# Optimization experiments

Measured on AMD Instinct MI355X. Metric: run time of the kernel, lower is better.

## Reference

```python
import jax, jax.numpy as jnp
import numpy as np

B, S, D_IN, D_OUT = 4, 2048, 1024, 1024

def setup_inputs() -> dict:
    key = jax.random.key(0)
    k0, k1, k2, k3 = jax.random.split(key, 4)
    sc = 1.0 / np.sqrt(D_IN)
    return {
        "x": jax.random.normal(k0, (B, S, D_IN), dtype=jnp.float32),
        "wq": jax.random.normal(k1, (D_OUT, D_IN), dtype=jnp.float32) * sc,
        "wk": jax.random.normal(k2, (D_OUT, D_IN), dtype=jnp.float32) * sc,
        "wv": jax.random.normal(k3, (D_OUT, D_IN), dtype=jnp.float32) * sc,
    }

def reference(x, wq, wk, wv):
    # Linear (no bias): y = x @ W.T, W shaped [d_out, d_in]
    q = jnp.einsum("bsd,ed->bse", x, wq)
    k = jnp.einsum("bsd,ed->bse", x, wk)
    v = jnp.einsum("bsd,ed->bse", x, wv)
    scores = jnp.einsum("bqe,bke->bqk", q, k)  # [B,S,S]
    n = x.shape[1]
    causal = jnp.triu(jnp.ones((n, n), dtype=bool), k=1)  # True above diagonal -> masked
    scores = jnp.where(causal, -jnp.inf, scores)
    attn = jax.nn.softmax(scores / jnp.sqrt(jnp.asarray(k.shape[-1], scores.dtype)), axis=-1)
    # dropout p=0.0 -> identity
    return jnp.einsum("bqk,bke->bqe", attn, v)
```

## Files before the change

### kernel.cpp

```cpp
#include <hip/hip_runtime.h>

#define Bb 4
#define Ss 2048
#define Dd 1024

typedef unsigned short u16;
typedef __bf16 bf16x8 __attribute__((ext_vector_type(8)));
typedef float  f32x4  __attribute__((ext_vector_type(4)));

__device__ inline u16 f2bf(float f) {
  union { float f; unsigned u; } x; x.f = f;
  unsigned u = x.u;
  return (u16)((u + 0x7fffu + ((u >> 16) & 1u)) >> 16);
}
__device__ inline float bf2f(u16 h) {
  union { unsigned u; float f; } x; x.u = ((unsigned)h) << 16;
  return x.f;
}

__device__ static inline void gl_lds16(const u16* g, u16* l) {
  __builtin_amdgcn_global_load_lds((__attribute__((address_space(1))) const void*)g,
                                   (__attribute__((address_space(3))) void*)l,
                                   16, 0, 0);
}

__device__ static inline void qbar() {
  asm volatile("" ::: "memory");
  __builtin_amdgcn_s_barrier();
  asm volatile("" ::: "memory");
}

template <int GATEN>
__device__ __forceinline__ void qk_gate() {
  if constexpr (GATEN == 5) asm volatile("s_waitcnt vmcnt(5)" ::: "memory");
  else if constexpr (GATEN == 0) asm volatile("s_waitcnt vmcnt(0)" ::: "memory");
}

__global__ __launch_bounds__(256) void cast_all(const float* __restrict__ x,
                                                const float* __restrict__ wq,
                                                const float* __restrict__ wk,
                                                const float* __restrict__ wv,
                                                u16* __restrict__ xb,
                                                u16* __restrict__ wb,
                                                float* __restrict__ lsum) {
  int id = blockIdx.x;
  if (id < 8) {
    float4 z = {0.f, 0.f, 0.f, 0.f};
    ((float4*)lsum)[id * 256 + threadIdx.x] = z;
  }
  const float* src; u16* dst; int off;
  if (id < 2048) {
    src = x; dst = xb; off = id * 4096;
  } else {
    int wi = id - 2048;
    int w = wi >> 8;
    src = (w == 0) ? wq : (w == 1) ? wk : wv;
    dst = wb + (size_t)w * Dd * Dd;
    off = (wi & 255) * 4096;
  }
#pragma unroll
  for (int t = 0; t < 4; t++) {
    int i = off + t * 1024 + threadIdx.x * 4;
    float4 v = *(const float4*)(src + i);
    unsigned p0 = (unsigned)f2bf(v.x) | ((unsigned)f2bf(v.y) << 16);
    unsigned p1 = (unsigned)f2bf(v.z) | ((unsigned)f2bf(v.w) << 16);
    uint2 p; p.x = p0; p.y = p1;
    *(uint2*)(dst + i) = p;
  }
}

#define BM 128
#define BN 128

__device__ inline void gemm_tile(const u16* __restrict__ A, int lda,
                                 const u16* __restrict__ Bp, int ldb,
                                 int kBeg, int kEnd,
                                 u16* lds, f32x4 acc[4][4]) {
  u16* lA0 = lds;
  u16* lB0 = lds + 4096;
  u16* lA1 = lds + 8192;
  u16* lB1 = lds + 12288;
  const int tid  = threadIdx.x;
  const int lane = tid & 63, wave = tid >> 6;
  const int quad = lane >> 4, r16 = lane & 15;
  const int wm = (wave & 1) * 64, wn = (wave >> 1) * 64;
  const int r0 = tid >> 2, part = tid & 3;

  for (int k0 = kBeg; k0 < kEnd; k0 += 64) {
    __syncthreads();
#pragma unroll
    for (int q = 0; q < 2; q++) {
      int row = q * 64 + r0;
      int s8 = (q * 256 + tid) * 8;
      const u16* ga = A  + (size_t)row * lda + k0 + part * 8;
      const u16* gb = Bp + (size_t)row * ldb + k0 + part * 8;
      gl_lds16(ga,      lA0 + s8);
      gl_lds16(gb,      lB0 + s8);
      gl_lds16(ga + 32, lA1 + s8);
      gl_lds16(gb + 32, lB1 + s8);
    }
    __syncthreads();
#pragma unroll
    for (int h = 0; h < 2; h++) {
      const u16* la = h ? lA1 : lA0;
      const u16* lb = h ? lB1 : lB0;
      bf16x8 fa[4], fb[4];
#pragma unroll
      for (int t = 0; t < 4; t++)
        fa[t] = *(const bf16x8*)(la + (wm + t * 16 + r16) * 32 + quad * 8);
#pragma unroll
      for (int t = 0; t < 4; t++)
        fb[t] = *(const bf16x8*)(lb + (wn + t * 16 + r16) * 32 + quad * 8);
#pragma unroll
      for (int tm = 0; tm < 4; tm++)
#pragma unroll
        for (int tn = 0; tn < 4; tn++)
          acc[tm][tn] = __builtin_amdgcn_mfma_f32_16x16x32_bf16(fa[tm], fb[tn],
                                                                acc[tm][tn], 0, 0, 0);
    }
  }
}

#define QBK 32
#define FBUF 20480

__global__ __launch_bounds__(512, 2) void qkv_fused(const u16* __restrict__ xb,
                                                    const u16* __restrict__ wb,
                                                    u16* __restrict__ qkv) {
  __shared__ __align__(16) u16 sh[3 * FBUF];

  const int id  = blockIdx.x;
  const int nt  = id & 7, mt = id >> 3;
  const int row0 = mt * 256, col0 = nt * 384;
  const u16* A  = xb + (size_t)row0 * Dd;
  const u16* Bp = wb + (size_t)col0 * Dd;

  const int tid  = threadIdx.x;
  const int lane = tid & 63, wave = tid >> 6;
  const int wr = wave >> 2, wc = wave & 3;
  const int quad = lane >> 4, r16 = lane & 15;

  const int rA0 = tid >> 2,          cA0 = tid & 3;
  const int rA1 = (tid + 512) >> 2,  cA1 = tid & 3;
  const int rB2 = (tid + 1024) >> 2;
  const u16* aS0 = A  + (size_t)rA0 * Dd + (size_t)((cA0 ^ ((rA0 >> 1) & 3)) * 8);
  const u16* aS1 = A  + (size_t)rA1 * Dd + (size_t)((cA1 ^ ((rA1 >> 1) & 3)) * 8);
  const u16* bS0 = Bp + (size_t)rA0 * Dd + (size_t)((cA0 ^ ((rA0 >> 1) & 3)) * 8);
  const u16* bS1 = Bp + (size_t)rA1 * Dd + (size_t)((cA1 ^ ((rA1 >> 1) & 3)) * 8);
  const u16* bS2 = Bp + (size_t)rB2 * Dd + (size_t)((cA0 ^ ((rB2 >> 1) & 3)) * 8);

  auto stg = [&](int S) {
    u16* d = sh + (S % 3) * FBUF;
    const size_t ko = (size_t)S * QBK;
    gl_lds16(aS0 + ko, d + tid * 8);
    gl_lds16(aS1 + ko, d + (tid + 512) * 8);
    u16* db = d + 8192;
    gl_lds16(bS0 + ko, db + tid * 8);
    gl_lds16(bS1 + ko, db + (tid + 512) * 8);
    gl_lds16(bS2 + ko, db + (tid + 1024) * 8);
  };

  const int chq  = (quad ^ ((r16 >> 1) & 3)) * 8;
  const int idxA = (wr * 128 + r16) * 32 + chq;
  const int idxB = 8192 + (wc * 96 + r16) * 32 + chq;

  f32x4 acc[8][6];
#pragma unroll
  for (int m = 0; m < 8; m++)
#pragma unroll
    for (int n = 0; n < 6; n++) acc[m][n] = (f32x4){0.f, 0.f, 0.f, 0.f};

#define FPH(T_, DOSTG, GATEN)                                                  \
  {                                                                            \
    const u16* bf = sh + ((T_) % 3) * FBUF;                                    \
    bf16x8 fb[6], fa[4];                                                       \
    _Pragma("unroll") for (int n = 0; n < 6; n++)                              \
        fb[n] = *(const bf16x8*)(bf + idxB + n * 512);                         \
    _Pragma("unroll") for (int m = 0; m < 4; m++)                              \
        fa[m] = *(const bf16x8*)(bf + idxA + m * 512);                         \
    if (DOSTG) stg((T_) + 2);                                                  \
    qk_gate<GATEN>();                                                          \
    qbar();                                                                    \
    __builtin_amdgcn_s_setprio(1);                                             \
    _Pragma("unroll") for (int m = 0; m < 4; m++)                              \
      _Pragma("unroll") for (int n = 0; n < 6; n++)                            \
        acc[m][n] = __builtin_amdgcn_mfma_f32_16x16x32_bf16(fa[m], fb[n],      \
                                                            acc[m][n], 0, 0, 0); \
    _Pragma("unroll") for (int m = 0; m < 4; m++)                              \
        fa[m] = *(const bf16x8*)(bf + idxA + (m + 4) * 512);                   \
    _Pragma("unroll") for (int m = 0; m < 4; m++)                              \
      _Pragma("unroll") for (int n = 0; n < 6; n++)                            \
        acc[m + 4][n] = __builtin_amdgcn_mfma_f32_16x16x32_bf16(fa[m], fb[n],  \
                                                                acc[m + 4][n], 0, 0, 0); \
    __builtin_amdgcn_s_setprio(0);                                             \
    qbar();                                                                    \
  }

  stg(0); stg(1);
  qk_gate<5>();
  qbar();

#pragma unroll 1
  for (int T = 0; T < 30; T++) FPH(T, true, 5);
  FPH(30, false, 0);
  FPH(31, false, -1);
#undef FPH

#pragma unroll
  for (int m = 0; m < 8; m++) {
    int rr = row0 + wr * 128 + m * 16 + quad * 4;
#pragma unroll
    for (int n = 0; n < 6; n++) {
      int cc = col0 + wc * 96 + n * 16 + r16;
      u16* o = qkv + (size_t)(cc >> 10) * ((size_t)Bb * Ss * Dd) + (cc & 1023);
#pragma unroll
      for (int r = 0; r < 4; r++)
        o[(size_t)(rr + r) * Dd] = f2bf(acc[m][n][r]);
    }
  }
}

__global__ __launch_bounds__(256) void scores_fused(const u16* __restrict__ qb,
                                                    const u16* __restrict__ kb,
                                                    const u16* __restrict__ vb,
                                                    u16* __restrict__ sc,
                                                    u16* __restrict__ vt,
                                                    float* __restrict__ lsum) {
  __shared__ __align__(16) u16 shmem[16384];
  const int id = blockIdx.x;
  const int tid = threadIdx.x;

  if (id >= 544) {
    const int bid = id - 544;
    u16 (*t)[72] = (u16(*)[72])shmem;
    for (int u = bid; u < 2048; u += 480) {
      const int b = u >> 9, rem = u & 511;
      const int e0 = (rem >> 5) * 64, s0 = (rem & 31) * 64;
      const u16* src = vb + (size_t)b * Ss * Dd;
      u16* dst = vt + (size_t)b * Dd * Ss;
      if (u != bid) __syncthreads();
#pragma unroll
      for (int gg = tid; gg < 512; gg += 256) {
        int row = gg >> 3, prt = gg & 7;
        uint4 v = *(const uint4*)(src + (size_t)(s0 + row) * Dd + e0 + prt * 8);
        const u16* pv = (const u16*)&v;
#pragma unroll
        for (int jj = 0; jj < 8; jj++) t[prt * 8 + jj][row] = pv[jj];
      }
      __syncthreads();
#pragma unroll
      for (int gg = tid; gg < 512; gg += 256) {
        int ee = gg >> 3, prt = gg & 7;
        uint4 v = *(const uint4*)(&t[ee][prt * 8]);
        *(uint4*)(dst + (size_t)(e0 + ee) * Ss + s0 + prt * 8) = v;
      }
    }
    return;
  }

  const int xcd = id & 7, j = id >> 3;
  const int b = j / 17, tloc = j - b * 17;
  const int t = xcd * 17 + tloc;
  int it = (int)((sqrtf(8.f * (float)t + 1.f) - 1.f) * 0.5f);
  while ((it + 1) * (it + 2) / 2 <= t) it++;
  while (it * (it + 1) / 2 > t) it--;
  const int jt = t - it * (it + 1) / 2;

  const u16* A  = qb + (size_t)b * Ss * Dd + (size_t)it * BM * Dd;
  const u16* Bp = kb + (size_t)b * Ss * Dd + (size_t)jt * BN * Dd;
  f32x4 acc[4][4];
  const f32x4 zero = {0.f, 0.f, 0.f, 0.f};
#pragma unroll
  for (int tm = 0; tm < 4; tm++)
#pragma unroll
    for (int tn = 0; tn < 4; tn++) acc[tm][tn] = zero;

  gemm_tile(A, Dd, Bp, Dd, 0, Dd, shmem, acc);

  u16* out = sc + (size_t)b * Ss * Ss;
  float* lr = lsum + (size_t)b * Ss;
  const int lane = tid & 63, wave = tid >> 6;
  const int quad = lane >> 4, r16 = lane & 15;
  const int wm = (wave & 1) * 64, wn = (wave >> 1) * 64;
#pragma unroll
  for (int tm = 0; tm < 4; tm++) {
    float psum[4] = {0.f, 0.f, 0.f, 0.f};
#pragma unroll
    for (int tn = 0; tn < 4; tn++) {
      int rr = it * BM + wm + tm * 16 + quad * 4;
      int cc = jt * BN + wn + tn * 16 + r16;
#pragma unroll
      for (int r = 0; r < 4; r++) {
        float p = 0.f;
        u16 h = 0;
        if (cc <= rr + r) {
          h = f2bf(__expf(acc[tm][tn][r] * 0.03125f));
          p = bf2f(h);
        }
        out[(size_t)(rr + r) * Ss + cc] = h;
        psum[r] += p;
      }
    }
#pragma unroll
    for (int r = 0; r < 4; r++) {
      float s = psum[r];
      s += __shfl_xor(s, 1);
      s += __shfl_xor(s, 2);
      s += __shfl_xor(s, 4);
      s += __shfl_xor(s, 8);
      if (r16 == 0) {
        int row = it * BM + wm + tm * 16 + quad * 4 + r;
        atomicAdd(&lr[row], s);
      }
    }
  }
}

__global__ __launch_bounds__(256) void pv_gemm(const u16* __restrict__ sc,
                                               const u16* __restrict__ vt,
                                               const float* __restrict__ lsum,
                                               float* __restrict__ out) {
  __shared__ __align__(16) u16 shmem[16384];
  const int idx = blockIdx.x;
  const int xcd = idx & 7, slot = idx >> 3;
  const int qp = slot >> 3, col = slot & 7;
  const int b = qp & 3;
  const int it = (qp >> 2) ? (15 - xcd) : xcd;
  const int row0 = it * BM;
  const int col0 = col * BN;
  const u16* A  = sc + (size_t)b * Ss * Ss + (size_t)row0 * Ss;
  const u16* Bp = vt + (size_t)b * Dd * Ss + (size_t)col0 * Ss;
  f32x4 acc[4][4];
  const f32x4 zero = {0.f, 0.f, 0.f, 0.f};
#pragma unroll
  for (int tm = 0; tm < 4; tm++)
#pragma unroll
    for (int tn = 0; tn < 4; tn++) acc[tm][tn] = zero;

  gemm_tile(A, Ss, Bp, Ss, 0, row0 + BM, shmem, acc);

  float* o = out + (size_t)b * Ss * Dd;
  const float* lr = lsum + (size_t)b * Ss;
  const int lane = threadIdx.x & 63, wave = threadIdx.x >> 6;
  const int quad = lane >> 4, r16 = lane & 15;
  const int wm = (wave & 1) * 64, wn = (wave >> 1) * 64;
#pragma unroll
  for (int tm = 0; tm < 4; tm++) {
    int rbase = row0 + wm + tm * 16 + quad * 4;
    float s0 = 1.f / lr[rbase], s1 = 1.f / lr[rbase + 1];
    float s2 = 1.f / lr[rbase + 2], s3 = 1.f / lr[rbase + 3];
#pragma unroll
    for (int tn = 0; tn < 4; tn++) {
      int cc = col0 + wn + tn * 16 + r16;
      o[(size_t)(rbase + 0) * Dd + cc] = acc[tm][tn][0] * s0;
      o[(size_t)(rbase + 1) * Dd + cc] = acc[tm][tn][1] * s1;
      o[(size_t)(rbase + 2) * Dd + cc] = acc[tm][tn][2] * s2;
      o[(size_t)(rbase + 3) * Dd + cc] = acc[tm][tn][3] * s3;
    }
  }
}

extern "C" void kernel_launch(void* const* d_in, const int* in_sizes, int n_in,
                              void* d_out, int out_size, void* d_ws, size_t ws_size,
                              hipStream_t stream) {
  const float* x  = (const float*)d_in[0];
  const float* wq = (const float*)d_in[1];
  const float* wk = (const float*)d_in[2];
  const float* wv = (const float*)d_in[3];
  float* out = (float*)d_out;
  char* ws = (char*)d_ws;
  if (ws_size < 106987520u) return;

  u16* qkv  = (u16*)(ws);
  u16* sc   = (u16*)(ws + 50331648u);
  u16* xb   = (u16*)(ws + 83886080u);
  u16* vt   = xb;
  u16* wb   = (u16*)(ws + 100663296u);
  float* lsum = (float*)(ws + 106954752u);

  const size_t nQ = (size_t)Bb * Ss * Dd;

  cast_all<<<2816, 256, 0, stream>>>(x, wq, wk, wv, xb, wb, lsum);
  qkv_fused<<<256, 512, 0, stream>>>(xb, wb, qkv);
  scores_fused<<<1024, 256, 0, stream>>>(qkv, qkv + nQ, qkv + 2 * nQ, sc, vt, lsum);
  pv_gemm<<<512, 256, 0, stream>>>(sc, vt, lsum, out);
}
```

Measured before the change: 242.8 us.

## Split QKV GEMM staging into separate A/B rings with staggered prefetch

Splits the single 3-stage LDS ring of the QKV projection GEMM into a 4-deep ring for the activation tile and a 3-deep ring for the weight tile. Each k-step is now two half-phases: the first issues the B prefetch and the second issues the A prefetch three steps ahead. The aim is to spread global-to-LDS loads across more barriers and keep more loads in flight, so the MFMA phases wait less on memory. In exchange the LDS footprint grows and launch bounds drop from 2 blocks to 1 block per CU, which lowers occupancy and adds an extra barrier per step.

After: 242.2 us. Within noise of the previous version (-0.2%).

```diff
diff --git a/kernel.cpp b/kernel.cpp
--- a/kernel.cpp
+++ b/kernel.cpp
@@ -32,7 +32,8 @@
 
 template <int GATEN>
 __device__ __forceinline__ void qk_gate() {
-  if constexpr (GATEN == 5) asm volatile("s_waitcnt vmcnt(5)" ::: "memory");
+  if constexpr (GATEN == 7) asm volatile("s_waitcnt vmcnt(7)" ::: "memory");
+  else if constexpr (GATEN == 5) asm volatile("s_waitcnt vmcnt(5)" ::: "memory");
   else if constexpr (GATEN == 0) asm volatile("s_waitcnt vmcnt(0)" ::: "memory");
 }
 
@@ -122,12 +123,13 @@
 }
 
 #define QBK 32
-#define FBUF 20480
-
-__global__ __launch_bounds__(512, 2) void qkv_fused(const u16* __restrict__ xb,
+#define ABUF 8192
+#define BBUF 12288
+
+__global__ __launch_bounds__(512, 1) void qkv_fused(const u16* __restrict__ xb,
                                                     const u16* __restrict__ wb,
                                                     u16* __restrict__ qkv) {
-  __shared__ __align__(16) u16 sh[3 * FBUF];
+  __shared__ __align__(16) u16 sh[4 * ABUF + 3 * BBUF];
 
   const int id  = blockIdx.x;
   const int nt  = id & 7, mt = id >> 3;
@@ -149,45 +151,59 @@
   const u16* bS1 = Bp + (size_t)rA1 * Dd + (size_t)((cA1 ^ ((rA1 >> 1) & 3)) * 8);
   const u16* bS2 = Bp + (size_t)rB2 * Dd + (size_t)((cA0 ^ ((rB2 >> 1) & 3)) * 8);
 
-  auto stg = [&](int S) {
-    u16* d = sh + (S % 3) * FBUF;
+  auto stgA = [&](int S) {
+    u16* d = sh + (S & 3) * ABUF;
     const size_t ko = (size_t)S * QBK;
     gl_lds16(aS0 + ko, d + tid * 8);
     gl_lds16(aS1 + ko, d + (tid + 512) * 8);
-    u16* db = d + 8192;
-    gl_lds16(bS0 + ko, db + tid * 8);
-    gl_lds16(bS1 + ko, db + (tid + 512) * 8);
-    gl_lds16(bS2 + ko, db + (tid + 1024) * 8);
+  };
+  auto stgB = [&](int S) {
+    u16* d = sh + 4 * ABUF + ((unsigned)S % 3u) * BBUF;
+    const size_t ko = (size_t)S * QBK;
+    gl_lds16(bS0 + ko, d + tid * 8);
+    gl_lds16(bS1 + ko, d + (tid + 512) * 8);
+    gl_lds16(bS2 + ko, d + (tid + 1024) * 8);
   };
 
   const int chq  = (quad ^ ((r16 >> 1) & 3)) * 8;
   const int idxA = (wr * 128 + r16) * 32 + chq;
-  const int idxB = 8192 + (wc * 96 + r16) * 32 + chq;
+  const int idxB = (wc * 96  + r16) * 32 + chq;
 
   f32x4 acc[8][6];
 #pragma unroll
   for (int m = 0; m < 8; m++)
 #pragma unroll
     for (int n = 0; n < 6; n++) acc[m][n] = (f32x4){0.f, 0.f, 0.f, 0.f};
-
-#define FPH(T_, DOSTG, GATEN)                                                  \
+  bf16x8 fb[6], fa[4];
+
+#define PH_A(T_, DOB)                                                          \
   {                                                                            \
-    const u16* bf = sh + ((T_) % 3) * FBUF;                                    \
-    bf16x8 fb[6], fa[4];                                                       \
+    const u16* lA = sh + ((T_) & 3) * ABUF;                                    \
+    const u16* lB = sh + 4 * ABUF + ((unsigned)(T_) % 3u) * BBUF;              \
     _Pragma("unroll") for (int n = 0; n < 6; n++)                              \
-        fb[n] = *(const bf16x8*)(bf + idxB + n * 512);                         \
+        fb[n] = *(const bf16x8*)(lB + idxB + n * 512);                         \
     _Pragma("unroll") for (int m = 0; m < 4; m++)                              \
-        fa[m] = *(const bf16x8*)(bf + idxA + m * 512);                         \
-    if (DOSTG) stg((T_) + 2);                                                  \
-    qk_gate<GATEN>();                                                          \
+        fa[m] = *(const bf16x8*)(lA + idxA + m * 512);                         \
+    if (DOB) stgB((T_) + 2);                                                   \
     qbar();                                                                    \
     __builtin_amdgcn_s_setprio(1);                                             \
     _Pragma("unroll") for (int m = 0; m < 4; m++)                              \
       _Pragma("unroll") for (int n = 0; n < 6; n++)                            \
         acc[m][n] = __builtin_amdgcn_mfma_f32_16x16x32_bf16(fa[m], fb[n],      \
                                                             acc[m][n], 0, 0, 0); \
+    __builtin_amdgcn_s_setprio(0);                                             \
+    qbar();                                                                    \
+  }
+
+#define PH_B(T_, DOA, GATEN)                                                   \
+  {                                                                            \
+    const u16* lA = sh + ((T_) & 3) * ABUF;                                    \
     _Pragma("unroll") for (int m = 0; m < 4; m++)                              \
-        fa[m] = *(const bf16x8*)(bf + idxA + (m + 4) * 512);                   \
+        fa[m] = *(const bf16x8*)(lA + idxA + (m + 4) * 512);                   \
+    if (DOA) stgA((T_) + 3);                                                   \
+    qk_gate<GATEN>();                                                          \
+    qbar();                                                                    \
+    __builtin_amdgcn_s_setprio(1);                                             \
     _Pragma("unroll") for (int m = 0; m < 4; m++)                              \
       _Pragma("unroll") for (int n = 0; n < 6; n++)                            \
         acc[m + 4][n] = __builtin_amdgcn_mfma_f32_16x16x32_bf16(fa[m], fb[n],  \
@@ -196,15 +212,17 @@
     qbar();                                                                    \
   }
 
-  stg(0); stg(1);
-  qk_gate<5>();
+  stgA(0); stgB(0); stgA(1); stgB(1); stgA(2);
+  qk_gate<7>();
   qbar();
 
 #pragma unroll 1
-  for (int T = 0; T < 30; T++) FPH(T, true, 5);
-  FPH(30, false, 0);
-  FPH(31, false, -1);
-#undef FPH
+  for (int T = 0; T < 29; T++) { PH_A(T, true) PH_B(T, true, 7) }
+  PH_A(29, true)  PH_B(29, false, 5)
+  PH_A(30, false) PH_B(30, false, 0)
+  PH_A(31, false) PH_B(31, false, -1)
+#undef PH_A
+#undef PH_B
 
 #pragma unroll
   for (int m = 0; m < 8; m++) {
```
